# Performance work log

Measured on AMD Instinct MI355X. Metric: run time of the kernel, lower is better.

The kernel has to match this reference:

```python
import jax, jax.numpy as jnp
import numpy as np

B, N, F_IN, F_OUT = 8, 2048, 256, 64
ALPHA = 0.2  # LeakyReLU negative slope
NEG_INF = -9e15


def setup_inputs() -> dict:
    key = jax.random.key(0)
    k1, k2, k3, k4 = jax.random.split(key, 4)
    h = jax.random.normal(k1, (B, N, F_IN), dtype=jnp.float32)
    adj = jax.random.randint(k2, (B, N, N), 0, 2, dtype=jnp.int32)
    W = jax.random.normal(k3, (F_IN, F_OUT), dtype=jnp.float32) * 0.1
    a = jax.random.normal(k4, (2 * F_OUT, 1), dtype=jnp.float32) * 0.1
    return {"h": h, "adj": adj, "W": W, "a": a}


def reference(h, adj, W, a):
    # Wh: [B, N, F_OUT]
    Wh = jnp.einsum('bnf,fo->bno', h, W)
    # Decompose the pairwise concat+MLP: e_ij = LeakyReLU(a1.Wh_i + a2.Wh_j)
    a1 = a[:F_OUT, 0]   # applied to source (row) node
    a2 = a[F_OUT:, 0]   # applied to target (col) node
    e_src = jnp.einsum('bno,o->bn', Wh, a1)  # [B, N]
    e_dst = jnp.einsum('bno,o->bn', Wh, a2)  # [B, N]
    e = jax.nn.leaky_relu(e_src[:, :, None] + e_dst[:, None, :], negative_slope=ALPHA)  # [B,N,N]
    e = jnp.where(adj > 0, e, NEG_INF)
    attention = jax.nn.softmax(e, axis=2)  # softmax over neighbors (dim=2)
    h_prime = jnp.einsum('bij,bjo->bio', attention, Wh)  # bmm
    return jax.nn.elu(h_prime)  # concat=True -> ELU
```

## Files before the change

### kernel.cpp

```cpp
#include <hip/hip_runtime.h>
#include <hip/hip_bf16.h>

#define B_ 8
#define N_ 2048
#define FIN 256
#define FOUT 64
#define BN_ (B_ * N_)
#define SEG 8
#define KSEG (N_ / SEG)
#define LDJ (KSEG + 8)
#define NEG_INF_F (-9.0e15f)

typedef unsigned short ushort_t;
typedef __attribute__((ext_vector_type(8))) __bf16 bf16x8;
typedef __attribute__((ext_vector_type(4))) float f32x4;

union U4B8 { uint4 u; bf16x8 b; };

__device__ __forceinline__ float lrelu(float x) { return fmaxf(x, 0.2f * x); }

__global__ __launch_bounds__(256) void k1_proj(
    const float* __restrict__ h, const float* __restrict__ W,
    const float* __restrict__ a, ushort_t* __restrict__ WhTB,
    float* __restrict__ e_src, float* __restrict__ e_dst)
{
    const int t = threadIdx.x;
    const int lane = t & 63;
    const int w = t >> 6;
    const int gr = blockIdx.x * 16 + w * 4;
    const int c = lane;
    const float* hrow = h + (size_t)gr * FIN;
    float v0 = 0.f, v1 = 0.f, v2 = 0.f, v3 = 0.f;
    for (int k = 0; k < FIN; k += 4) {
        const float4 h0 = *(const float4*)(hrow + k);
        const float4 h1 = *(const float4*)(hrow + FIN + k);
        const float4 h2 = *(const float4*)(hrow + 2 * FIN + k);
        const float4 h3 = *(const float4*)(hrow + 3 * FIN + k);
        const float w0 = W[(k + 0) * FOUT + c];
        const float w1 = W[(k + 1) * FOUT + c];
        const float w2 = W[(k + 2) * FOUT + c];
        const float w3 = W[(k + 3) * FOUT + c];
        v0 += h0.x * w0 + h0.y * w1 + h0.z * w2 + h0.w * w3;
        v1 += h1.x * w0 + h1.y * w1 + h1.z * w2 + h1.w * w3;
        v2 += h2.x * w0 + h2.y * w1 + h2.z * w2 + h2.w * w3;
        v3 += h3.x * w0 + h3.y * w1 + h3.z * w2 + h3.w * w3;
    }
    const float a1c = a[c], a2c = a[FOUT + c];
    float s10 = v0 * a1c, s11 = v1 * a1c, s12 = v2 * a1c, s13 = v3 * a1c;
    float s20 = v0 * a2c, s21 = v1 * a2c, s22 = v2 * a2c, s23 = v3 * a2c;
    for (int off = 32; off; off >>= 1) {
        s10 += __shfl_xor(s10, off); s11 += __shfl_xor(s11, off);
        s12 += __shfl_xor(s12, off); s13 += __shfl_xor(s13, off);
        s20 += __shfl_xor(s20, off); s21 += __shfl_xor(s21, off);
        s22 += __shfl_xor(s22, off); s23 += __shfl_xor(s23, off);
    }
    if (lane == 0) {
        *(float4*)(e_src + gr) = make_float4(s10, s11, s12, s13);
        *(float4*)(e_dst + gr) = make_float4(s20, s21, s22, s23);
    }
    const int b = gr >> 11, i = gr & (N_ - 1);
    ushort4 us;
    us.x = __builtin_bit_cast(unsigned short, (__bf16)v0);
    us.y = __builtin_bit_cast(unsigned short, (__bf16)v1);
    us.z = __builtin_bit_cast(unsigned short, (__bf16)v2);
    us.w = __builtin_bit_cast(unsigned short, (__bf16)v3);
    *(ushort4*)(WhTB + (size_t)(b * FOUT + c) * N_ + i) = us;
}

__global__ __launch_bounds__(256) void k3_attn(
    const int* __restrict__ adj, const ushort_t* __restrict__ WhTB,
    const float* __restrict__ e_src, const float* __restrict__ e_dst,
    float* __restrict__ s_buf, float* __restrict__ partial)
{
    __shared__ ushort_t WhT[FOUT * LDJ];
    __shared__ float edl[KSEG];
    const int t = threadIdx.x;
    const int lane = t & 63, wid = t >> 6;
    const int b = blockIdx.x >> 4, tg = blockIdx.x & 15;
    const int seg = blockIdx.y;
    const int jseg = seg * KSEG;

    #pragma unroll
    for (int it = 0; it < 8; ++it) {
        const int chunk = it * 256 + t;
        const int cc = chunk >> 5, j8 = (chunk & 31) * 8;
        *(uint4*)(&WhT[cc * LDJ + j8]) =
            *(const uint4*)(WhTB + (size_t)(b * FOUT + cc) * N_ + jseg + j8);
    }
    if (t < 64) *(float4*)(&edl[t * 4]) = *(const float4*)(e_dst + b * N_ + jseg + t * 4);
    __syncthreads();

    const int l15 = lane & 15, g = lane >> 4;
    const int i0 = (tg * 4 + wid) * 32;
    const int rlo = b * N_ + i0 + l15;
    const int rhi = rlo + 16;
    const int* adj_lo = adj + (size_t)rlo * N_ + jseg;
    const int* adj_hi = adj + (size_t)rhi * N_ + jseg;
    const float es_lo = e_src[rlo], es_hi = e_src[rhi];

    f32x4 acc[2][4];
    #pragma unroll
    for (int m = 0; m < 2; ++m)
        #pragma unroll
        for (int n = 0; n < 4; ++n)
            #pragma unroll
            for (int r = 0; r < 4; ++r) acc[m][n][r] = 0.f;

    float slo = 0.f, shi = 0.f;

    for (int kc = 0; kc < KSEG; kc += 32) {
        const int jl = kc + g * 8;
        const int4 alo0 = *(const int4*)(adj_lo + jl);
        const int4 alo1 = *(const int4*)(adj_lo + jl + 4);
        const int4 ahi0 = *(const int4*)(adj_hi + jl);
        const int4 ahi1 = *(const int4*)(adj_hi + jl + 4);
        const float4 ed0 = *(const float4*)(&edl[jl]);
        const float4 ed1 = *(const float4*)(&edl[jl + 4]);
        const float ev[8] = {ed0.x, ed0.y, ed0.z, ed0.w, ed1.x, ed1.y, ed1.z, ed1.w};
        const int alo[8] = {alo0.x, alo0.y, alo0.z, alo0.w, alo1.x, alo1.y, alo1.z, alo1.w};
        const int ahi[8] = {ahi0.x, ahi0.y, ahi0.z, ahi0.w, ahi1.x, ahi1.y, ahi1.z, ahi1.w};
        bf16x8 aflo, afhi;
        #pragma unroll
        for (int u = 0; u < 8; ++u) {
            float e0 = lrelu(es_lo + ev[u]);
            e0 = alo[u] > 0 ? e0 : NEG_INF_F;
            const float p0 = __expf(e0);
            slo += p0;
            aflo[u] = (__bf16)p0;
            float e1 = lrelu(es_hi + ev[u]);
            e1 = ahi[u] > 0 ? e1 : NEG_INF_F;
            const float p1 = __expf(e1);
            shi += p1;
            afhi[u] = (__bf16)p1;
        }
        #pragma unroll
        for (int n = 0; n < 4; ++n) {
            U4B8 bfr;
            bfr.u = *(const uint4*)(&WhT[(n * 16 + l15) * LDJ + jl]);
            acc[0][n] = __builtin_amdgcn_mfma_f32_16x16x32_bf16(aflo, bfr.b, acc[0][n], 0, 0, 0);
            acc[1][n] = __builtin_amdgcn_mfma_f32_16x16x32_bf16(afhi, bfr.b, acc[1][n], 0, 0, 0);
        }
    }
    slo += __shfl_xor(slo, 16); slo += __shfl_xor(slo, 32);
    shi += __shfl_xor(shi, 16); shi += __shfl_xor(shi, 32);
    if (lane < 16) {
        atomicAdd(&s_buf[b * N_ + i0 + lane], slo);
        atomicAdd(&s_buf[b * N_ + i0 + 16 + lane], shi);
    }
    const size_t base = ((size_t)seg * BN_ + b * N_ + i0) * FOUT;
    #pragma unroll
    for (int m = 0; m < 2; ++m)
        #pragma unroll
        for (int n = 0; n < 4; ++n)
            #pragma unroll
            for (int r = 0; r < 4; ++r) {
                const int row = m * 16 + g * 4 + r;
                const int col = n * 16 + l15;
                partial[base + (size_t)row * FOUT + col] = acc[m][n][r];
            }
}

__global__ __launch_bounds__(256) void k4_out(
    const float* __restrict__ partial, const float* __restrict__ s_buf,
    float* __restrict__ out)
{
    const int gid = blockIdx.x * 256 + threadIdx.x;
    const int bi = gid >> 4, c4 = (gid & 15) * 4;
    float4 s = make_float4(0.f, 0.f, 0.f, 0.f);
    #pragma unroll
    for (int seg = 0; seg < SEG; ++seg) {
        const float4 v = *(const float4*)(partial + ((size_t)seg * BN_ + bi) * FOUT + c4);
        s.x += v.x; s.y += v.y; s.z += v.z; s.w += v.w;
    }
    const float rs = 1.0f / s_buf[bi];
    float4 o; float x;
    x = s.x * rs; o.x = x > 0.f ? x : __expf(x) - 1.f;
    x = s.y * rs; o.y = x > 0.f ? x : __expf(x) - 1.f;
    x = s.z * rs; o.z = x > 0.f ? x : __expf(x) - 1.f;
    x = s.w * rs; o.w = x > 0.f ? x : __expf(x) - 1.f;
    *(float4*)(out + (size_t)bi * FOUT + c4) = o;
}

extern "C" void kernel_launch(void* const* d_in, const int* in_sizes, int n_in,
                              void* d_out, int out_size, void* d_ws, size_t ws_size,
                              hipStream_t stream) {
    const float* h = (const float*)d_in[0];
    const int* adj = (const int*)d_in[1];
    const float* W = (const float*)d_in[2];
    const float* a = (const float*)d_in[3];
    float* out = (float*)d_out;

    char* ws = (char*)d_ws;
    ushort_t* WhTB = (ushort_t*)ws;
    float* e_src = (float*)(ws + 2 * 1024 * 1024);
    float* e_dst = e_src + BN_;
    float* s_buf = e_dst + BN_;
    float* partial = s_buf + BN_;

    hipMemsetAsync(s_buf, 0, BN_ * sizeof(float), stream);
    k1_proj<<<BN_ / 16, 256, 0, stream>>>(h, W, a, WhTB, e_src, e_dst);
    k3_attn<<<dim3(128, SEG), 256, 0, stream>>>(adj, WhTB, e_src, e_dst, s_buf, partial);
    k4_out<<<BN_ * 16 / 256, 256, 0, stream>>>(partial, s_buf, out);
}
```

Before: 277.2 us.

## Fuse attention split-K reduction and output into one kernel with in-block reduction

Restructures the attention kernel so each 512-thread block owns 16 rows and its 8 waves each cover a 256-column slice of the neighbor dimension, with partial outputs and row sums reduced in shared memory. This removes the partial-buffer round trip, the atomics, the memset and the separate output kernel. Each wave now reads Wh fragments directly from global memory instead of staging them in LDS, and prefetches the next adjacency chunk into registers. The trade-off is more global/L2 traffic for Wh and e_dst (reused from cache), and a block-wide reduction with barriers at the end.

```diff
diff --git a/kernel.cpp b/kernel.cpp
--- a/kernel.cpp
+++ b/kernel.cpp
@@ -6,18 +6,13 @@
 #define FIN 256
 #define FOUT 64
 #define BN_ (B_ * N_)
-#define SEG 8
-#define KSEG (N_ / SEG)
-#define LDJ (KSEG + 8)
-#define NEG_INF_F (-9.0e15f)
+#define KSEG 256
 
 typedef unsigned short ushort_t;
 typedef __attribute__((ext_vector_type(8))) __bf16 bf16x8;
 typedef __attribute__((ext_vector_type(4))) float f32x4;
 
 union U4B8 { uint4 u; bf16x8 b; };
-
-__device__ __forceinline__ float lrelu(float x) { return fmaxf(x, 0.2f * x); }
 
 __global__ __launch_bounds__(256) void k1_proj(
     const float* __restrict__ h, const float* __restrict__ W,
@@ -67,118 +62,103 @@
     *(ushort4*)(WhTB + (size_t)(b * FOUT + c) * N_ + i) = us;
 }
 
-__global__ __launch_bounds__(256) void k3_attn(
+__global__ __launch_bounds__(512, 4) void k3_attn(
     const int* __restrict__ adj, const ushort_t* __restrict__ WhTB,
     const float* __restrict__ e_src, const float* __restrict__ e_dst,
-    float* __restrict__ s_buf, float* __restrict__ partial)
+    float* __restrict__ out)
 {
-    __shared__ ushort_t WhT[FOUT * LDJ];
-    __shared__ float edl[KSEG];
+    __shared__ float red[8 * 16 * 68];
+    __shared__ float sred[8 * 16];
+    __shared__ float ssum[16];
+
     const int t = threadIdx.x;
     const int lane = t & 63, wid = t >> 6;
-    const int b = blockIdx.x >> 4, tg = blockIdx.x & 15;
-    const int seg = blockIdx.y;
-    const int jseg = seg * KSEG;
+    const int l15 = lane & 15, g = lane >> 4;
+    const int b = blockIdx.x & 7;
+    const int tile = blockIdx.x >> 3;
+    const int i0 = tile * 16;
+    const int jseg = wid * KSEG;
 
+    const size_t row_g = (size_t)(b * N_ + i0 + l15);
+    const int* arow = adj + row_g * N_ + jseg + g * 8;
+    const float* edp = e_dst + b * N_ + jseg + g * 8;
+    const ushort_t* wb = WhTB + (size_t)(b * FOUT + l15) * N_ + jseg + g * 8;
+    const float es = e_src[row_g];
+
+    f32x4 acc[4];
     #pragma unroll
-    for (int it = 0; it < 8; ++it) {
-        const int chunk = it * 256 + t;
-        const int cc = chunk >> 5, j8 = (chunk & 31) * 8;
-        *(uint4*)(&WhT[cc * LDJ + j8]) =
-            *(const uint4*)(WhTB + (size_t)(b * FOUT + cc) * N_ + jseg + j8);
-    }
-    if (t < 64) *(float4*)(&edl[t * 4]) = *(const float4*)(e_dst + b * N_ + jseg + t * 4);
-    __syncthreads();
+    for (int n = 0; n < 4; ++n)
+        #pragma unroll
+        for (int r = 0; r < 4; ++r) acc[n][r] = 0.f;
+    float srow = 0.f;
 
-    const int l15 = lane & 15, g = lane >> 4;
-    const int i0 = (tg * 4 + wid) * 32;
-    const int rlo = b * N_ + i0 + l15;
-    const int rhi = rlo + 16;
-    const int* adj_lo = adj + (size_t)rlo * N_ + jseg;
-    const int* adj_hi = adj + (size_t)rhi * N_ + jseg;
-    const float es_lo = e_src[rlo], es_hi = e_src[rhi];
-
-    f32x4 acc[2][4];
+    int4 c0 = *(const int4*)(arow);
+    int4 c1 = *(const int4*)(arow + 4);
     #pragma unroll
-    for (int m = 0; m < 2; ++m)
-        #pragma unroll
-        for (int n = 0; n < 4; ++n)
-            #pragma unroll
-            for (int r = 0; r < 4; ++r) acc[m][n][r] = 0.f;
-
-    float slo = 0.f, shi = 0.f;
-
     for (int kc = 0; kc < KSEG; kc += 32) {
-        const int jl = kc + g * 8;
-        const int4 alo0 = *(const int4*)(adj_lo + jl);
-        const int4 alo1 = *(const int4*)(adj_lo + jl + 4);
-        const int4 ahi0 = *(const int4*)(adj_hi + jl);
-        const int4 ahi1 = *(const int4*)(adj_hi + jl + 4);
-        const float4 ed0 = *(const float4*)(&edl[jl]);
-        const float4 ed1 = *(const float4*)(&edl[jl + 4]);
+        int4 p0, p1;
+        if (kc + 32 < KSEG) {
+            p0 = *(const int4*)(arow + kc + 32);
+            p1 = *(const int4*)(arow + kc + 36);
+        } else { p0 = c0; p1 = c1; }
+        const float4 ed0 = *(const float4*)(edp + kc);
+        const float4 ed1 = *(const float4*)(edp + kc + 4);
         const float ev[8] = {ed0.x, ed0.y, ed0.z, ed0.w, ed1.x, ed1.y, ed1.z, ed1.w};
-        const int alo[8] = {alo0.x, alo0.y, alo0.z, alo0.w, alo1.x, alo1.y, alo1.z, alo1.w};
-        const int ahi[8] = {ahi0.x, ahi0.y, ahi0.z, ahi0.w, ahi1.x, ahi1.y, ahi1.z, ahi1.w};
-        bf16x8 aflo, afhi;
+        const int aa[8] = {c0.x, c0.y, c0.z, c0.w, c1.x, c1.y, c1.z, c1.w};
+        bf16x8 af;
         #pragma unroll
         for (int u = 0; u < 8; ++u) {
-            float e0 = lrelu(es_lo + ev[u]);
-            e0 = alo[u] > 0 ? e0 : NEG_INF_F;
-            const float p0 = __expf(e0);
-            slo += p0;
-            aflo[u] = (__bf16)p0;
-            float e1 = lrelu(es_hi + ev[u]);
-            e1 = ahi[u] > 0 ? e1 : NEG_INF_F;
-            const float p1 = __expf(e1);
-            shi += p1;
-            afhi[u] = (__bf16)p1;
+            float e = es + ev[u];
+            e = fmaxf(e, 0.2f * e);
+            const float p = aa[u] > 0 ? __expf(e) : 0.f;
+            srow += p;
+            af[u] = (__bf16)p;
         }
         #pragma unroll
         for (int n = 0; n < 4; ++n) {
             U4B8 bfr;
-            bfr.u = *(const uint4*)(&WhT[(n * 16 + l15) * LDJ + jl]);
-            acc[0][n] = __builtin_amdgcn_mfma_f32_16x16x32_bf16(aflo, bfr.b, acc[0][n], 0, 0, 0);
-            acc[1][n] = __builtin_amdgcn_mfma_f32_16x16x32_bf16(afhi, bfr.b, acc[1][n], 0, 0, 0);
+            bfr.u = *(const uint4*)(wb + (size_t)n * 16 * N_ + kc);
+            acc[n] = __builtin_amdgcn_mfma_f32_16x16x32_bf16(af, bfr.b, acc[n], 0, 0, 0);
+        }
+        c0 = p0; c1 = p1;
+    }
+
+    srow += __shfl_xor(srow, 16);
+    srow += __shfl_xor(srow, 32);
+    if (lane < 16) sred[wid * 16 + lane] = srow;
+
+    #pragma unroll
+    for (int n = 0; n < 4; ++n)
+        #pragma unroll
+        for (int r = 0; r < 4; ++r)
+            red[(wid * 16 + g * 4 + r) * 68 + n * 16 + l15] = acc[n][r];
+    __syncthreads();
+
+    if (t < 16) {
+        float s = 0.f;
+        #pragma unroll
+        for (int w = 0; w < 8; ++w) s += sred[w * 16 + t];
+        ssum[t] = 1.0f / s;
+    }
+    const int row = t >> 4, c4 = (t & 15) * 4;
+    float4 v = make_float4(0.f, 0.f, 0.f, 0.f);
+    if (t < 256) {
+        #pragma unroll
+        for (int w = 0; w < 8; ++w) {
+            const float4 u = *(const float4*)&red[(w * 16 + row) * 68 + c4];
+            v.x += u.x; v.y += u.y; v.z += u.z; v.w += u.w;
         }
     }
-    slo += __shfl_xor(slo, 16); slo += __shfl_xor(slo, 32);
-    shi += __shfl_xor(shi, 16); shi += __shfl_xor(shi, 32);
-    if (lane < 16) {
-        atomicAdd(&s_buf[b * N_ + i0 + lane], slo);
-        atomicAdd(&s_buf[b * N_ + i0 + 16 + lane], shi);
+    __syncthreads();
+    if (t < 256) {
+        const float rs = ssum[row];
+        float4 o; float x;
+        x = v.x * rs; o.x = x > 0.f ? x : __expf(x) - 1.f;
+        x = v.y * rs; o.y = x > 0.f ? x : __expf(x) - 1.f;
+        x = v.z * rs; o.z = x > 0.f ? x : __expf(x) - 1.f;
+        x = v.w * rs; o.w = x > 0.f ? x : __expf(x) - 1.f;
+        *(float4*)(out + ((size_t)(b * N_ + i0 + row)) * FOUT + c4) = o;
     }
-    const size_t base = ((size_t)seg * BN_ + b * N_ + i0) * FOUT;
-    #pragma unroll
-    for (int m = 0; m < 2; ++m)
-        #pragma unroll
-        for (int n = 0; n < 4; ++n)
-            #pragma unroll
-            for (int r = 0; r < 4; ++r) {
-                const int row = m * 16 + g * 4 + r;
-                const int col = n * 16 + l15;
-                partial[base + (size_t)row * FOUT + col] = acc[m][n][r];
-            }
-}
-
-__global__ __launch_bounds__(256) void k4_out(
-    const float* __restrict__ partial, const float* __restrict__ s_buf,
-    float* __restrict__ out)
-{
-    const int gid = blockIdx.x * 256 + threadIdx.x;
-    const int bi = gid >> 4, c4 = (gid & 15) * 4;
-    float4 s = make_float4(0.f, 0.f, 0.f, 0.f);
-    #pragma unroll
-    for (int seg = 0; seg < SEG; ++seg) {
-        const float4 v = *(const float4*)(partial + ((size_t)seg * BN_ + bi) * FOUT + c4);
-        s.x += v.x; s.y += v.y; s.z += v.z; s.w += v.w;
-    }
-    const float rs = 1.0f / s_buf[bi];
-    float4 o; float x;
-    x = s.x * rs; o.x = x > 0.f ? x : __expf(x) - 1.f;
-    x = s.y * rs; o.y = x > 0.f ? x : __expf(x) - 1.f;
-    x = s.z * rs; o.z = x > 0.f ? x : __expf(x) - 1.f;
-    x = s.w * rs; o.w = x > 0.f ? x : __expf(x) - 1.f;
-    *(float4*)(out + (size_t)bi * FOUT + c4) = o;
 }
 
 extern "C" void kernel_launch(void* const* d_in, const int* in_sizes, int n_in,
@@ -194,11 +174,7 @@
     ushort_t* WhTB = (ushort_t*)ws;
     float* e_src = (float*)(ws + 2 * 1024 * 1024);
     float* e_dst = e_src + BN_;
-    float* s_buf = e_dst + BN_;
-    float* partial = s_buf + BN_;
 
-    hipMemsetAsync(s_buf, 0, BN_ * sizeof(float), stream);
     k1_proj<<<BN_ / 16, 256, 0, stream>>>(h, W, a, WhTB, e_src, e_dst);
-    k3_attn<<<dim3(128, SEG), 256, 0, stream>>>(adj, WhTB, e_src, e_dst, s_buf, partial);
-    k4_out<<<BN_ * 16 / 256, 256, 0, stream>>>(partial, s_buf, out);
+    k3_attn<<<BN_ / 16, 512, 0, stream>>>(adj, WhTB, e_src, e_dst, out);
 }
```

Result: faster. 270.7 us (-2.3%).
